# Performance work log

Measured on AMD Instinct MI355X. Metric: run time of the kernel, lower is better.

## Reference

```python
import jax, jax.numpy as jnp
import numpy as np

B, H, S, DK = 2, 16, 2048, 64

def setup_inputs() -> dict:
    key = jax.random.key(0)
    kq, kk, kv, km = jax.random.split(key, 4)
    queries = jax.random.normal(kq, (B, H, S, DK), dtype=jnp.float32)
    keys = jax.random.normal(kk, (B, H, S, DK), dtype=jnp.float32)
    values = jax.random.normal(kv, (B, H, S, DK), dtype=jnp.float32)
    mask = jax.random.randint(km, (B, S, S), 0, 2, dtype=jnp.int32)
    return {"queries": queries, "keys": keys, "values": values, "mask": mask}

def reference(queries, keys, values, mask):
    d_k = queries.shape[-1]
    scale = 1.0 / np.sqrt(d_k).astype(np.float32)
    # [B,H,S,S]
    scores = jnp.einsum('bhqd,bhkd->bhqk', queries, keys) * scale
    m = mask[:, None, :, :]  # broadcast over heads, like mask.unsqueeze(1)
    scores = jnp.where(m == 0, jnp.asarray(-1e9, scores.dtype), scores)
    attn = jax.nn.softmax(scores, axis=-1)
    return jnp.einsum('bhqk,bhkd->bhqd', attn, values)
```

## Files before the change

### kernel.cpp

```cpp
#include <hip/hip_runtime.h>


#define S_   2048
#define D_   64
#define H_   16
#define B_   2
#define BH_  32
#define KVB  64
#define NKV  (S_/KVB)
#define QPB  128
#define NQT  (S_/QPB)

#define KSCALE 0.18033688f

typedef __attribute__((ext_vector_type(8)))  _Float16 f16x8;
typedef __attribute__((ext_vector_type(4)))  _Float16 f16x4;
typedef __attribute__((ext_vector_type(2)))  _Float16 f16x2;
typedef __attribute__((ext_vector_type(4)))  float    f32x4;
typedef __attribute__((ext_vector_type(16))) float    f32x16;
typedef __attribute__((ext_vector_type(4)))  unsigned u32x4;

static __device__ __forceinline__ void async16(const void* g, void* l) {
  __builtin_amdgcn_global_load_lds(
      (const __attribute__((address_space(1))) void*)g,
      (__attribute__((address_space(3))) void*)l, 16, 0, 0);
}

static __device__ __forceinline__ f16x2 pkrtz(float a, float b) {
  return __builtin_bit_cast(f16x2, __builtin_amdgcn_cvt_pkrtz(a, b));
}

static __device__ __forceinline__ void plswap(unsigned& a, unsigned& b, int h) {
#if __has_builtin(__builtin_amdgcn_permlane32_swap)
  auto r = __builtin_amdgcn_permlane32_swap(a, b, false, false);
  a = (unsigned)r[0];
  b = (unsigned)r[1];
#else
  unsigned sa = __shfl_xor(a, 32), sb = __shfl_xor(b, 32);
  unsigned na = h ? sb : a, nb = h ? b : sa;
  a = na; b = nb;
#endif
}

__global__ __launch_bounds__(256) void prepass_k(
    const float* __restrict__ K, const float* __restrict__ V,
    const int* __restrict__ M,
    _Float16* __restrict__ Kh, _Float16* __restrict__ Vth,
    unsigned long long* __restrict__ Mb) {
  __shared__ float tile[64][65];
  const int bidx = blockIdx.x;
  const int tid = threadIdx.x;
  if (bidx < 1024) {
    int st = bidx & 31;
    int bh = bidx >> 5;
    const float* src = V + ((size_t)bh * S_ + st * 64) * D_;
    int r = tid >> 2, cq = tid & 3;
#pragma unroll
    for (int j = 0; j < 4; ++j) {
      float4 v = ((const float4*)(src + (size_t)r * D_))[cq + 4 * j];
      int col = (cq + 4 * j) * 4;
      tile[r][col + 0] = v.x; tile[r][col + 1] = v.y;
      tile[r][col + 2] = v.z; tile[r][col + 3] = v.w;
    }
    __syncthreads();
    int d = tid >> 2, s = (tid & 3) * 16;
    _Float16 tmp[16];
#pragma unroll
    for (int j = 0; j < 16; ++j) tmp[j] = (_Float16)tile[s + j][d];
    _Float16* dstp = Vth + ((size_t)bh * D_ + d) * S_ + st * 64 + s;
    *(f16x8*)(dstp)     = *((f16x8*)tmp);
    *(f16x8*)(dstp + 8) = *((f16x8*)tmp + 1);
  } else if (bidx < 1536) {
    int idx = (bidx - 1024) * 256 + tid;
#pragma unroll
    for (int j = 0; j < 8; ++j) {
      int i = idx + j * 131072;
      float4 v = ((const float4*)K)[i];
      f16x4 o = {(_Float16)(v.x * KSCALE), (_Float16)(v.y * KSCALE),
                 (_Float16)(v.z * KSCALE), (_Float16)(v.w * KSCALE)};
      *(f16x4*)(Kh + 4 * (size_t)i) = o;
    }
  } else {
    int lane = tid & 63;
    int wb = (bidx - 1536) * 256 + (tid >> 6) * 64;
    for (int i = 0; i < 64; ++i) {
      int w = wb + i;
      int m = M[(size_t)w * 64 + lane];
      unsigned long long bal = __ballot(m != 0);
      if (lane == 0) Mb[w] = bal;
    }
  }
}

__global__ __launch_bounds__(256, 2) void attn_fwd(
    const float* __restrict__ Qf, const _Float16* __restrict__ Kh,
    const _Float16* __restrict__ Vth, const unsigned long long* __restrict__ Mb,
    float* __restrict__ Out) {
  __shared__ _Float16 Kt[2][KVB * D_];
  __shared__ _Float16 Vt[2][D_ * KVB];
  __shared__ unsigned long long MLUT[16];

  const int tid = threadIdx.x;
  const int lane = tid & 63;
  const int wid = tid >> 6;
  const int h = lane >> 5;
  const int c5 = lane & 31;
  const int c7 = c5 & 7;

  if (tid < 16) {
    unsigned w0 = ((tid & 1) ? 0x3C00u : 0u) | ((tid & 2) ? 0x3C000000u : 0u);
    unsigned w1 = ((tid & 4) ? 0x3C00u : 0u) | ((tid & 8) ? 0x3C000000u : 0u);
    MLUT[tid] = (unsigned long long)w0 | ((unsigned long long)w1 << 32);
  }

  int bid = blockIdx.x;
  bid = (bid & 7) * 64 + (bid >> 3);
  const int qt = bid & (NQT - 1);
  const int bh = bid >> 4;
  const int b = bh >> 4;

  const int q = qt * QPB + wid * 32 + c5;

  f16x8 qf[4];
  {
    const float* qp = Qf + ((size_t)bh * S_ + q) * D_ + 8 * h;
#pragma unroll
    for (int dc = 0; dc < 4; ++dc) {
      _Float16 t[8];
#pragma unroll
      for (int j = 0; j < 8; ++j) t[j] = (_Float16)qp[16 * dc + j];
      qf[dc] = *(f16x8*)t;
    }
  }

  f32x16 accO0, accO1;
#pragma unroll
  for (int e = 0; e < 16; ++e) { accO0[e] = 0.f; accO1[e] = 0.f; }
  float m_run = -INFINITY, l_run = 0.f;

  const _Float16* kbase = Kh + (size_t)bh * S_ * D_;
  const _Float16* vbase = Vth + (size_t)bh * D_ * S_;
  const unsigned long long* pmb = Mb + ((size_t)b * S_ + q) * NKV;
  const f16x2 one2 = {(_Float16)1.0f, (_Float16)1.0f};

#define STAGE(buf, kvi)                                                     \
  {                                                                         \
    _Pragma("unroll") for (int it = 0; it < 2; ++it) {                      \
      int gid = it * 256 + tid;                                             \
      int row = gid >> 3, gr = gid & 7;                                     \
      int gs = (gr ^ (row & 7)) << 3;                                       \
      int ldso = ((gid & ~63) * 8);                                         \
      async16(kbase + ((size_t)((kvi)*KVB + row)) * D_ + gs, &Kt[buf][ldso]); \
      async16(vbase + (size_t)row * S_ + (kvi)*KVB + gs, &Vt[buf][ldso]);   \
    }                                                                       \
  }

  STAGE(0, 0);

#pragma unroll 2
  for (int kv = 0; kv < NKV; ++kv) {
    const int cur = kv & 1;
    __syncthreads();
    unsigned long long mw = pmb[kv];
    if (kv + 1 < NKV) STAGE(cur ^ 1, kv + 1);

    const _Float16* Ktc = Kt[cur];
    const _Float16* Vtc = Vt[cur];

    f32x16 st0, st1;
#pragma unroll
    for (int e = 0; e < 16; ++e) { st0[e] = 0.f; st1[e] = 0.f; }
    __builtin_amdgcn_s_setprio(1);
#pragma unroll
    for (int dc = 0; dc < 4; ++dc) {
      int slot = (((2 * dc + h) ^ c7) << 3);
      f16x8 k0 = *(const f16x8*)(&Ktc[(c5)      * D_ + slot]);
      f16x8 k1 = *(const f16x8*)(&Ktc[(32 + c5) * D_ + slot]);
      st0 = __builtin_amdgcn_mfma_f32_32x32x16_f16(k0, qf[dc], st0, 0, 0, 0);
      st1 = __builtin_amdgcn_mfma_f32_32x32x16_f16(k1, qf[dc], st1, 0, 0, 0);
    }
    __builtin_amdgcn_s_setprio(0);

    float pmax = -INFINITY;
#pragma unroll
    for (int e = 0; e < 16; ++e) {
      pmax = fmaxf(pmax, st0[e]);
      pmax = fmaxf(pmax, st1[e]);
    }
    pmax = fmaxf(pmax, __shfl_xor(pmax, 32));
    if (!__all(pmax - m_run <= 8.f)) {
      float mn = fmaxf(m_run, pmax);
      float cf = __builtin_amdgcn_exp2f(m_run - mn);
      l_run *= cf;
#pragma unroll
      for (int e = 0; e < 16; ++e) { accO0[e] *= cf; accO1[e] *= cf; }
      m_run = mn;
    }

    float rs = 0.f;
    unsigned pkd[2][4][2];
#pragma unroll
    for (int kt = 0; kt < 2; ++kt) {
#pragma unroll
      for (int rr = 0; rr < 4; ++rr) {
        int n = 8 * kt + 2 * rr + h;
        unsigned nib = (unsigned)(mw >> (4 * n)) & 0xFu;
        unsigned long long lut = MLUT[nib];
        f16x2 m01 = __builtin_bit_cast(f16x2, (unsigned)lut);
        f16x2 m23 = __builtin_bit_cast(f16x2, (unsigned)(lut >> 32));
        float e0 = (kt ? st1[4 * rr + 0] : st0[4 * rr + 0]) - m_run;
        float e1 = (kt ? st1[4 * rr + 1] : st0[4 * rr + 1]) - m_run;
        float e2 = (kt ? st1[4 * rr + 2] : st0[4 * rr + 2]) - m_run;
        float e3 = (kt ? st1[4 * rr + 3] : st0[4 * rr + 3]) - m_run;
        f16x2 p0 = pkrtz(__builtin_amdgcn_exp2f(e0), __builtin_amdgcn_exp2f(e1)) * m01;
        f16x2 p1 = pkrtz(__builtin_amdgcn_exp2f(e2), __builtin_amdgcn_exp2f(e3)) * m23;
        rs = __builtin_amdgcn_fdot2(p0, one2, rs, false);
        rs = __builtin_amdgcn_fdot2(p1, one2, rs, false);
        pkd[kt][rr][0] = __builtin_bit_cast(unsigned, p0);
        pkd[kt][rr][1] = __builtin_bit_cast(unsigned, p1);
      }
    }
    rs += __shfl_xor(rs, 32);
    l_run += rs;

    f16x8 pfrag[4];
#pragma unroll
    for (int kc = 0; kc < 4; ++kc) {
      int jl = 2 * kc, jh = 2 * kc + 1;
      unsigned a0 = pkd[jl >> 2][jl & 3][0], a1 = pkd[jl >> 2][jl & 3][1];
      unsigned b0 = pkd[jh >> 2][jh & 3][0], b1 = pkd[jh >> 2][jh & 3][1];
      plswap(a0, b0, h);
      plswap(a1, b1, h);
      u32x4 fr = {a0, a1, b0, b1};
      pfrag[kc] = __builtin_bit_cast(f16x8, fr);
    }

    __builtin_amdgcn_s_setprio(1);
#pragma unroll
    for (int kc = 0; kc < 4; ++kc) {
      int slot = (((2 * kc + h) ^ c7) << 3);
      f16x8 v0 = *(const f16x8*)(&Vtc[(c5)      * KVB + slot]);
      f16x8 v1 = *(const f16x8*)(&Vtc[(32 + c5) * KVB + slot]);
      accO0 = __builtin_amdgcn_mfma_f32_32x32x16_f16(v0, pfrag[kc], accO0, 0, 0, 0);
      accO1 = __builtin_amdgcn_mfma_f32_32x32x16_f16(v1, pfrag[kc], accO1, 0, 0, 0);
    }
    __builtin_amdgcn_s_setprio(0);
  }

  float inv = 1.0f / l_run;
  float* op = Out + ((size_t)bh * S_ + q) * D_;
#pragma unroll
  for (int rr = 0; rr < 4; ++rr) {
    f32x4 o0, o1;
#pragma unroll
    for (int e = 0; e < 4; ++e) {
      o0[e] = accO0[4 * rr + e] * inv;
      o1[e] = accO1[4 * rr + e] * inv;
    }
    *(f32x4*)(op + 8 * rr + 4 * h)      = o0;
    *(f32x4*)(op + 32 + 8 * rr + 4 * h) = o1;
  }
}

extern "C" void kernel_launch(void* const* d_in, const int* in_sizes, int n_in,
                              void* d_out, int out_size, void* d_ws, size_t ws_size,
                              hipStream_t stream) {
  const float* Q = (const float*)d_in[0];
  const float* K = (const float*)d_in[1];
  const float* V = (const float*)d_in[2];
  const int*   M = (const int*)d_in[3];
  float* Out = (float*)d_out;

  const size_t NE = (size_t)B_ * H_ * S_ * D_;
  _Float16* Kh  = (_Float16*)d_ws;
  _Float16* Vth = Kh + NE;
  unsigned long long* Mb = (unsigned long long*)(Vth + NE);

  prepass_k<<<2048, 256, 0, stream>>>(K, V, M, Kh, Vth, Mb);
  attn_fwd<<<NQT * BH_, 256, 0, stream>>>(Q, Kh, Vth, Mb, Out);
}
```

Measured before the change: 192.6 us.

## Split KV range across two wave groups per block and merge softmax partials

Doubles the block to 512 threads, with two groups of four waves that process alternating KV tiles for the same 128 queries. The two groups' online-softmax partial states are combined through shared memory at the end. The aim is more waves in flight per block, hiding latency, while keeping the grid size unchanged. The cost is twice the shared-memory staging per block, an extra cross-group merge with barriers, and higher register pressure under the new launch bounds.

After: 190.6 us. No clear change (-1.1%).

```diff
diff --git a/kernel.cpp b/kernel.cpp
--- a/kernel.cpp
+++ b/kernel.cpp
@@ -8,6 +8,7 @@
 #define BH_  32
 #define KVB  64
 #define NKV  (S_/KVB)
+#define NRND (NKV/2)
 #define QPB  128
 #define NQT  (S_/QPB)
 
@@ -92,17 +93,19 @@
   }
 }
 
-__global__ __launch_bounds__(256, 2) void attn_fwd(
+__global__ __launch_bounds__(512, 4) void attn_fwd(
     const float* __restrict__ Qf, const _Float16* __restrict__ Kh,
     const _Float16* __restrict__ Vth, const unsigned long long* __restrict__ Mb,
     float* __restrict__ Out) {
-  __shared__ _Float16 Kt[2][KVB * D_];
-  __shared__ _Float16 Vt[2][D_ * KVB];
+  __shared__ _Float16 Kt[2][2][KVB * D_];
+  __shared__ _Float16 Vt[2][2][D_ * KVB];
   __shared__ unsigned long long MLUT[16];
 
   const int tid = threadIdx.x;
   const int lane = tid & 63;
   const int wid = tid >> 6;
+  const int p = wid & 3;
+  const int half = wid >> 2;
   const int h = lane >> 5;
   const int c5 = lane & 31;
   const int c7 = c5 & 7;
@@ -119,7 +122,7 @@
   const int bh = bid >> 4;
   const int b = bh >> 4;
 
-  const int q = qt * QPB + wid * 32 + c5;
+  const int q = qt * QPB + p * 32 + c5;
 
   f16x8 qf[4];
   {
@@ -138,34 +141,35 @@
   for (int e = 0; e < 16; ++e) { accO0[e] = 0.f; accO1[e] = 0.f; }
   float m_run = -INFINITY, l_run = 0.f;
 
-  const _Float16* kbase = Kh + (size_t)bh * S_ * D_;
-  const _Float16* vbase = Vth + (size_t)bh * D_ * S_;
+  const int srow = tid >> 3, sgr = tid & 7;
+  const int gs = (sgr ^ (srow & 7)) << 3;
+  const _Float16* kp = Kh + (size_t)bh * S_ * D_ + (size_t)srow * D_ + gs;
+  const _Float16* vp = Vth + (size_t)bh * D_ * S_ + (size_t)srow * S_ + gs;
+  const int ldso = (tid & ~63) * 8;
   const unsigned long long* pmb = Mb + ((size_t)b * S_ + q) * NKV;
   const f16x2 one2 = {(_Float16)1.0f, (_Float16)1.0f};
 
-#define STAGE(buf, kvi)                                                     \
-  {                                                                         \
-    _Pragma("unroll") for (int it = 0; it < 2; ++it) {                      \
-      int gid = it * 256 + tid;                                             \
-      int row = gid >> 3, gr = gid & 7;                                     \
-      int gs = (gr ^ (row & 7)) << 3;                                       \
-      int ldso = ((gid & ~63) * 8);                                         \
-      async16(kbase + ((size_t)((kvi)*KVB + row)) * D_ + gs, &Kt[buf][ldso]); \
-      async16(vbase + (size_t)row * S_ + (kvi)*KVB + gs, &Vt[buf][ldso]);   \
-    }                                                                       \
-  }
-
-  STAGE(0, 0);
+#define STAGE1(set, par, t)                                          \
+  {                                                                  \
+    async16(kp + (size_t)(t) * (KVB * D_), &Kt[set][par][ldso]);     \
+    async16(vp + (size_t)(t) * KVB,        &Vt[set][par][ldso]);     \
+  }
+
+  STAGE1(0, 0, 0);
+  STAGE1(0, 1, 1);
 
 #pragma unroll 2
-  for (int kv = 0; kv < NKV; ++kv) {
-    const int cur = kv & 1;
+  for (int r = 0; r < NRND; ++r) {
+    const int cur = r & 1;
     __syncthreads();
-    unsigned long long mw = pmb[kv];
-    if (kv + 1 < NKV) STAGE(cur ^ 1, kv + 1);
-
-    const _Float16* Ktc = Kt[cur];
-    const _Float16* Vtc = Vt[cur];
+    unsigned long long mw = pmb[2 * r + half];
+    if (r + 1 < NRND) {
+      STAGE1(cur ^ 1, 0, 2 * r + 2);
+      STAGE1(cur ^ 1, 1, 2 * r + 3);
+    }
+
+    const _Float16* Ktc = Kt[cur][half];
+    const _Float16* Vtc = Vt[cur][half];
 
     f32x16 st0, st1;
 #pragma unroll
@@ -247,18 +251,39 @@
     __builtin_amdgcn_s_setprio(0);
   }
 
-  float inv = 1.0f / l_run;
-  float* op = Out + ((size_t)bh * S_ + q) * D_;
-#pragma unroll
-  for (int rr = 0; rr < 4; ++rr) {
-    f32x4 o0, o1;
-#pragma unroll
-    for (int e = 0; e < 4; ++e) {
-      o0[e] = accO0[4 * rr + e] * inv;
-      o1[e] = accO1[4 * rr + e] * inv;
-    }
-    *(f32x4*)(op + 8 * rr + 4 * h)      = o0;
-    *(f32x4*)(op + 32 + 8 * rr + 4 * h) = o1;
+  __syncthreads();
+  {
+    float* cbA = (float*)&Kt[0][0][0];
+    float* cbB = (float*)&Vt[0][0][0];
+    if (half) {
+      float* da = cbA + (p * 64 + lane) * 17;
+      float* db = cbB + (p * 64 + lane) * 17;
+#pragma unroll
+      for (int e = 0; e < 16; ++e) { da[e] = accO0[e]; db[e] = accO1[e]; }
+      da[16] = m_run; db[16] = l_run;
+    }
+    __syncthreads();
+    if (!half) {
+      const float* sa = cbA + (p * 64 + lane) * 17;
+      const float* sb = cbB + (p * 64 + lane) * 17;
+      float m_b = sa[16], l_b = sb[16];
+      float m = fmaxf(m_run, m_b);
+      float ca  = __builtin_amdgcn_exp2f(m_run - m);
+      float cb2 = __builtin_amdgcn_exp2f(m_b - m);
+      float inv = 1.0f / (l_run * ca + l_b * cb2);
+      float* op = Out + ((size_t)bh * S_ + q) * D_;
+#pragma unroll
+      for (int rr = 0; rr < 4; ++rr) {
+        f32x4 o0, o1;
+#pragma unroll
+        for (int e = 0; e < 4; ++e) {
+          o0[e] = (accO0[4 * rr + e] * ca + sa[4 * rr + e] * cb2) * inv;
+          o1[e] = (accO1[4 * rr + e] * ca + sb[4 * rr + e] * cb2) * inv;
+        }
+        *(f32x4*)(op + 8 * rr + 4 * h)      = o0;
+        *(f32x4*)(op + 32 + 8 * rr + 4 * h) = o1;
+      }
+    }
   }
 }
 
@@ -277,5 +302,5 @@
   unsigned long long* Mb = (unsigned long long*)(Vth + NE);
 
   prepass_k<<<2048, 256, 0, stream>>>(K, V, M, Kh, Vth, Mb);
-  attn_fwd<<<NQT * BH_, 256, 0, stream>>>(Q, Kh, Vth, Mb, Out);
-}
+  attn_fwd<<<NQT * BH_, 512, 0, stream>>>(Q, Kh, Vth, Mb, Out);
+}
```

## Software-pipeline QK^T of next tile with softmax/PV, triple-buffer K/V

Applied to the files above, without the earlier changes.

Moves from double to triple-buffered K/V tiles in LDS, prefetching two tiles ahead. The QK^T MFMAs for tile R+1 are issued before the softmax and PV of tile R, with alternating score register sets, so matrix-core work can overlap the exp/mask ALU work. The mask word is also prefetched one iteration early. The row max becomes a tree reduction and the row sum uses two accumulators to shorten dependency chains. In exchange it needs 50% more LDS per block and roughly 32 more accumulator VGPRs, which may hurt occupancy or cause spills.

Measured after the change: 192.2 us. No clear change (-0.3%).

```diff
diff --git a/kernel.cpp b/kernel.cpp
--- a/kernel.cpp
+++ b/kernel.cpp
@@ -96,13 +96,12 @@
     const float* __restrict__ Qf, const _Float16* __restrict__ Kh,
     const _Float16* __restrict__ Vth, const unsigned long long* __restrict__ Mb,
     float* __restrict__ Out) {
-  __shared__ _Float16 Kt[2][KVB * D_];
-  __shared__ _Float16 Vt[2][D_ * KVB];
+  __shared__ _Float16 Ks[3][KVB * D_];
+  __shared__ _Float16 Vs[3][D_ * KVB];
   __shared__ unsigned long long MLUT[16];
 
   const int tid = threadIdx.x;
   const int lane = tid & 63;
-  const int wid = tid >> 6;
   const int h = lane >> 5;
   const int c5 = lane & 31;
   const int c7 = c5 & 7;
@@ -119,7 +118,7 @@
   const int bh = bid >> 4;
   const int b = bh >> 4;
 
-  const int q = qt * QPB + wid * 32 + c5;
+  const int q = qt * QPB + (tid >> 6) * 32 + c5;
 
   f16x8 qf[4];
   {
@@ -138,113 +137,133 @@
   for (int e = 0; e < 16; ++e) { accO0[e] = 0.f; accO1[e] = 0.f; }
   float m_run = -INFINITY, l_run = 0.f;
 
-  const _Float16* kbase = Kh + (size_t)bh * S_ * D_;
-  const _Float16* vbase = Vth + (size_t)bh * D_ * S_;
+  const int srow = tid >> 3, sgr = tid & 7;
+  const int gs = (sgr ^ (srow & 7)) << 3;
+  const _Float16* kp = Kh + (size_t)bh * S_ * D_ + (size_t)srow * D_ + gs;
+  const _Float16* vp = Vth + (size_t)bh * D_ * S_ + (size_t)srow * S_ + gs;
+  const int ldso = (tid & ~63) * 8;
   const unsigned long long* pmb = Mb + ((size_t)b * S_ + q) * NKV;
   const f16x2 one2 = {(_Float16)1.0f, (_Float16)1.0f};
 
-#define STAGE(buf, kvi)                                                     \
+  _Float16 *Kc = &Ks[0][0], *Kn = &Ks[1][0], *Kf = &Ks[2][0];
+  _Float16 *Vc = &Vs[0][0], *Vn = &Vs[1][0], *Vf = &Vs[2][0];
+
+#define STAGE(KB, VB, t)                                                    \
   {                                                                         \
-    _Pragma("unroll") for (int it = 0; it < 2; ++it) {                      \
-      int gid = it * 256 + tid;                                             \
-      int row = gid >> 3, gr = gid & 7;                                     \
-      int gs = (gr ^ (row & 7)) << 3;                                       \
-      int ldso = ((gid & ~63) * 8);                                         \
-      async16(kbase + ((size_t)((kvi)*KVB + row)) * D_ + gs, &Kt[buf][ldso]); \
-      async16(vbase + (size_t)row * S_ + (kvi)*KVB + gs, &Vt[buf][ldso]);   \
-    }                                                                       \
-  }
-
-  STAGE(0, 0);
-
-#pragma unroll 2
-  for (int kv = 0; kv < NKV; ++kv) {
-    const int cur = kv & 1;
-    __syncthreads();
-    unsigned long long mw = pmb[kv];
-    if (kv + 1 < NKV) STAGE(cur ^ 1, kv + 1);
-
-    const _Float16* Ktc = Kt[cur];
-    const _Float16* Vtc = Vt[cur];
-
-    f32x16 st0, st1;
-#pragma unroll
-    for (int e = 0; e < 16; ++e) { st0[e] = 0.f; st1[e] = 0.f; }
-    __builtin_amdgcn_s_setprio(1);
-#pragma unroll
-    for (int dc = 0; dc < 4; ++dc) {
-      int slot = (((2 * dc + h) ^ c7) << 3);
-      f16x8 k0 = *(const f16x8*)(&Ktc[(c5)      * D_ + slot]);
-      f16x8 k1 = *(const f16x8*)(&Ktc[(32 + c5) * D_ + slot]);
-      st0 = __builtin_amdgcn_mfma_f32_32x32x16_f16(k0, qf[dc], st0, 0, 0, 0);
-      st1 = __builtin_amdgcn_mfma_f32_32x32x16_f16(k1, qf[dc], st1, 0, 0, 0);
-    }
-    __builtin_amdgcn_s_setprio(0);
-
-    float pmax = -INFINITY;
-#pragma unroll
-    for (int e = 0; e < 16; ++e) {
-      pmax = fmaxf(pmax, st0[e]);
-      pmax = fmaxf(pmax, st1[e]);
-    }
-    pmax = fmaxf(pmax, __shfl_xor(pmax, 32));
-    if (!__all(pmax - m_run <= 8.f)) {
-      float mn = fmaxf(m_run, pmax);
-      float cf = __builtin_amdgcn_exp2f(m_run - mn);
-      l_run *= cf;
-#pragma unroll
-      for (int e = 0; e < 16; ++e) { accO0[e] *= cf; accO1[e] *= cf; }
-      m_run = mn;
-    }
-
-    float rs = 0.f;
-    unsigned pkd[2][4][2];
-#pragma unroll
-    for (int kt = 0; kt < 2; ++kt) {
-#pragma unroll
-      for (int rr = 0; rr < 4; ++rr) {
-        int n = 8 * kt + 2 * rr + h;
-        unsigned nib = (unsigned)(mw >> (4 * n)) & 0xFu;
-        unsigned long long lut = MLUT[nib];
-        f16x2 m01 = __builtin_bit_cast(f16x2, (unsigned)lut);
-        f16x2 m23 = __builtin_bit_cast(f16x2, (unsigned)(lut >> 32));
-        float e0 = (kt ? st1[4 * rr + 0] : st0[4 * rr + 0]) - m_run;
-        float e1 = (kt ? st1[4 * rr + 1] : st0[4 * rr + 1]) - m_run;
-        float e2 = (kt ? st1[4 * rr + 2] : st0[4 * rr + 2]) - m_run;
-        float e3 = (kt ? st1[4 * rr + 3] : st0[4 * rr + 3]) - m_run;
-        f16x2 p0 = pkrtz(__builtin_amdgcn_exp2f(e0), __builtin_amdgcn_exp2f(e1)) * m01;
-        f16x2 p1 = pkrtz(__builtin_amdgcn_exp2f(e2), __builtin_amdgcn_exp2f(e3)) * m23;
-        rs = __builtin_amdgcn_fdot2(p0, one2, rs, false);
-        rs = __builtin_amdgcn_fdot2(p1, one2, rs, false);
-        pkd[kt][rr][0] = __builtin_bit_cast(unsigned, p0);
-        pkd[kt][rr][1] = __builtin_bit_cast(unsigned, p1);
-      }
-    }
-    rs += __shfl_xor(rs, 32);
-    l_run += rs;
-
-    f16x8 pfrag[4];
-#pragma unroll
-    for (int kc = 0; kc < 4; ++kc) {
-      int jl = 2 * kc, jh = 2 * kc + 1;
-      unsigned a0 = pkd[jl >> 2][jl & 3][0], a1 = pkd[jl >> 2][jl & 3][1];
-      unsigned b0 = pkd[jh >> 2][jh & 3][0], b1 = pkd[jh >> 2][jh & 3][1];
-      plswap(a0, b0, h);
-      plswap(a1, b1, h);
-      u32x4 fr = {a0, a1, b0, b1};
-      pfrag[kc] = __builtin_bit_cast(f16x8, fr);
-    }
-
-    __builtin_amdgcn_s_setprio(1);
-#pragma unroll
-    for (int kc = 0; kc < 4; ++kc) {
-      int slot = (((2 * kc + h) ^ c7) << 3);
-      f16x8 v0 = *(const f16x8*)(&Vtc[(c5)      * KVB + slot]);
-      f16x8 v1 = *(const f16x8*)(&Vtc[(32 + c5) * KVB + slot]);
-      accO0 = __builtin_amdgcn_mfma_f32_32x32x16_f16(v0, pfrag[kc], accO0, 0, 0, 0);
-      accO1 = __builtin_amdgcn_mfma_f32_32x32x16_f16(v1, pfrag[kc], accO1, 0, 0, 0);
-    }
-    __builtin_amdgcn_s_setprio(0);
+    async16(kp + (size_t)(t) * (KVB * D_),            (KB) + ldso);         \
+    async16(kp + (size_t)(t) * (KVB * D_) + 32 * D_,  (KB) + ldso + 2048);  \
+    async16(vp + (size_t)(t) * KVB,                   (VB) + ldso);         \
+    async16(vp + (size_t)(t) * KVB + (size_t)32 * S_, (VB) + ldso + 2048);  \
+  }
+
+#define QKT(S0, S1, KB)                                                     \
+  {                                                                         \
+    _Pragma("unroll") for (int e = 0; e < 16; ++e) { S0[e] = 0.f; S1[e] = 0.f; } \
+    __builtin_amdgcn_s_setprio(1);                                          \
+    _Pragma("unroll") for (int dc = 0; dc < 4; ++dc) {                      \
+      int slot = (((2 * dc + h) ^ c7) << 3);                                \
+      f16x8 k0 = *(const f16x8*)(&(KB)[(c5)*D_ + slot]);                    \
+      f16x8 k1 = *(const f16x8*)(&(KB)[(32 + c5) * D_ + slot]);             \
+      S0 = __builtin_amdgcn_mfma_f32_32x32x16_f16(k0, qf[dc], S0, 0, 0, 0); \
+      S1 = __builtin_amdgcn_mfma_f32_32x32x16_f16(k1, qf[dc], S1, 0, 0, 0); \
+    }                                                                       \
+    __builtin_amdgcn_s_setprio(0);                                          \
+  }
+
+#define SOFTMAX_PV(S0, S1, VB, MW)                                          \
+  {                                                                         \
+                                           \
+    float t16[16];                                                          \
+    _Pragma("unroll") for (int e = 0; e < 16; ++e)                          \
+        t16[e] = fmaxf(S0[e], S1[e]);                                       \
+    _Pragma("unroll") for (int e = 0; e < 8; ++e)                           \
+        t16[e] = fmaxf(t16[e], t16[e + 8]);                                 \
+    _Pragma("unroll") for (int e = 0; e < 4; ++e)                           \
+        t16[e] = fmaxf(t16[e], t16[e + 4]);                                 \
+    float pmax = fmaxf(fmaxf(t16[0], t16[1]), fmaxf(t16[2], t16[3]));       \
+    pmax = fmaxf(pmax, __shfl_xor(pmax, 32));                               \
+    if (!__all(pmax - m_run <= 8.f)) {                                      \
+      float mn = fmaxf(m_run, pmax);                                        \
+      float cf = __builtin_amdgcn_exp2f(m_run - mn);                        \
+      l_run *= cf;                                                          \
+      _Pragma("unroll") for (int e = 0; e < 16; ++e) {                      \
+        accO0[e] *= cf; accO1[e] *= cf;                                     \
+      }                                                                     \
+      m_run = mn;                                                           \
+    }                                                                       \
+    float rs0 = 0.f, rs1 = 0.f;                                             \
+    unsigned pkd[2][4][2];                                                  \
+    _Pragma("unroll") for (int kt = 0; kt < 2; ++kt) {                      \
+      _Pragma("unroll") for (int rr = 0; rr < 4; ++rr) {                    \
+        int n = 8 * kt + 2 * rr + h;                                        \
+        unsigned nib = (unsigned)((MW) >> (4 * n)) & 0xFu;                  \
+        unsigned long long lut = MLUT[nib];                                 \
+        f16x2 m01 = __builtin_bit_cast(f16x2, (unsigned)lut);               \
+        f16x2 m23 = __builtin_bit_cast(f16x2, (unsigned)(lut >> 32));       \
+        float e0 = (kt ? S1[4 * rr + 0] : S0[4 * rr + 0]) - m_run;          \
+        float e1 = (kt ? S1[4 * rr + 1] : S0[4 * rr + 1]) - m_run;          \
+        float e2 = (kt ? S1[4 * rr + 2] : S0[4 * rr + 2]) - m_run;          \
+        float e3 = (kt ? S1[4 * rr + 3] : S0[4 * rr + 3]) - m_run;          \
+        f16x2 p0 = pkrtz(__builtin_amdgcn_exp2f(e0),                        \
+                         __builtin_amdgcn_exp2f(e1)) * m01;                 \
+        f16x2 p1 = pkrtz(__builtin_amdgcn_exp2f(e2),                        \
+                         __builtin_amdgcn_exp2f(e3)) * m23;                 \
+        rs0 = __builtin_amdgcn_fdot2(p0, one2, rs0, false);                 \
+        rs1 = __builtin_amdgcn_fdot2(p1, one2, rs1, false);                 \
+        pkd[kt][rr][0] = __builtin_bit_cast(unsigned, p0);                  \
+        pkd[kt][rr][1] = __builtin_bit_cast(unsigned, p1);                  \
+      }                                                                     \
+    }                                                                       \
+    float rs = rs0 + rs1;                                                   \
+    rs += __shfl_xor(rs, 32);                                               \
+    l_run += rs;                                                            \
+    f16x8 pfrag[4];                                                         \
+    _Pragma("unroll") for (int kc = 0; kc < 4; ++kc) {                      \
+      int jl = 2 * kc, jh = 2 * kc + 1;                                     \
+      unsigned a0 = pkd[jl >> 2][jl & 3][0], a1 = pkd[jl >> 2][jl & 3][1];  \
+      unsigned b0 = pkd[jh >> 2][jh & 3][0], b1 = pkd[jh >> 2][jh & 3][1];  \
+      plswap(a0, b0, h);                                                    \
+      plswap(a1, b1, h);                                                    \
+      u32x4 fr = {a0, a1, b0, b1};                                          \
+      pfrag[kc] = __builtin_bit_cast(f16x8, fr);                            \
+    }                                                                       \
+    __builtin_amdgcn_s_setprio(1);                                          \
+    _Pragma("unroll") for (int kc = 0; kc < 4; ++kc) {                      \
+      int slot = (((2 * kc + h) ^ c7) << 3);                                \
+      f16x8 v0 = *(const f16x8*)(&(VB)[(c5)*KVB + slot]);                   \
+      f16x8 v1 = *(const f16x8*)(&(VB)[(32 + c5) * KVB + slot]);            \
+      accO0 = __builtin_amdgcn_mfma_f32_32x32x16_f16(v0, pfrag[kc], accO0, 0, 0, 0); \
+      accO1 = __builtin_amdgcn_mfma_f32_32x32x16_f16(v1, pfrag[kc], accO1, 0, 0, 0); \
+    }                                                                       \
+    __builtin_amdgcn_s_setprio(0);                                          \
+  }
+
+#define ROTATE()                                                            \
+  { _Float16* t1 = Kc; Kc = Kn; Kn = Kf; Kf = t1;                           \
+    _Float16* t2 = Vc; Vc = Vn; Vn = Vf; Vf = t2; }
+
+#define BODY(R, SC0, SC1, SN0, SN1)                                         \
+  {                                                                         \
+    __syncthreads();                    \
+    unsigned long long mw = mw_next;                                        \
+    if ((R) + 1 < NKV) mw_next = pmb[(R) + 1];                              \
+    if ((R) + 2 < NKV) STAGE(Kf, Vf, (R) + 2);                              \
+    if ((R) + 1 < NKV) QKT(SN0, SN1, Kn);          \
+    SOFTMAX_PV(SC0, SC1, Vc, mw);               \
+    ROTATE();                                                               \
+  }
+
+  f32x16 stA0, stA1, stB0, stB1;
+
+  unsigned long long mw_next = pmb[0];
+  STAGE(Kc, Vc, 0);
+  STAGE(Kn, Vn, 1);
+  __syncthreads();
+  QKT(stA0, stA1, Kc);
+
+  for (int k2 = 0; k2 < NKV / 2; ++k2) {
+    BODY(2 * k2,     stA0, stA1, stB0, stB1);
+    BODY(2 * k2 + 1, stB0, stB1, stA0, stA1);
   }
 
   float inv = 1.0f / l_run;
```
